# Optimization experiments

Measured on AMD Instinct MI355X. Metric: run time of the kernel, lower is better.

## Reference

```python
import jax, jax.numpy as jnp
import numpy as np
from jax import lax

WINDOW = 144
N_ROUNDS = 1
REDUCTION = 4
RES_SCALE = 0.1


def conv2d(x, w, b, pad):
    # x: (N,C,H,W), w: (O,I,kh,kw)
    out = lax.conv_general_dilated(x, w, (1, 1), [(pad, pad), (pad, pad)],
                                   dimension_numbers=('NCHW', 'OIHW', 'NCHW'))
    return out + b[None, :, None, None]


def l2norm(x, eps):
    # matches torch F.normalize: x / clamp_min(||x||, eps)
    n = jnp.sqrt(jnp.sum(x * x, axis=-1, keepdims=True))
    return x / jnp.maximum(n, eps)


def _adjacent(t):
    # t: (N, rounds, k, w, e) -> concat [self, roll+1, roll-1] along window dim
    back = jnp.roll(t, 1, axis=2)
    fwd = jnp.roll(t, -1, axis=2)
    return jnp.concatenate([t, back, fwd], axis=3)


def _forward(input_x, w_match, b_match, w_asm, b_asm, means):
    N, C, H, W = input_x.shape
    L = H * W
    Cr = C // REDUCTION
    x_embed = conv2d(input_x, w_match, b_match, 1).reshape(N, Cr, L).transpose(0, 2, 1)  # (N,L,Cr)
    y_embed = conv2d(input_x, w_asm, b_asm, 0).reshape(N, C, L).transpose(0, 2, 1)       # (N,L,C)

    # ---- k-means bucket routing (no-grad in original) ----
    xn = jnp.broadcast_to(l2norm(x_embed, 1e-12)[:, None], (N, N_ROUNDS, L, Cr))
    dists = jnp.einsum('bhld,hcd->bhlc', lax.stop_gradient(xn), means)
    buckets = jnp.argmax(dists, axis=-1)                      # (N, rounds, L)
    n_clusters = means.shape[1]
    offsets = (jnp.arange(N_ROUNDS) * n_clusters)[None, :, None]
    codes = (buckets + offsets).reshape(N, N_ROUNDS * L)

    # ---- sort tokens by bucket code, gather embeddings ----
    indices = jnp.argsort(codes, axis=-1)
    undo_sort = jnp.argsort(indices, axis=-1)
    mod_idx = indices % L
    x_sorted = jnp.take_along_axis(x_embed, mod_idx[..., None], axis=1)  # (N, r*L, Cr)
    y_sorted = jnp.take_along_axis(y_embed, mod_idx[..., None], axis=1)  # (N, r*L, C)

    padding = (WINDOW - L % WINDOW) % WINDOW
    xb = x_sorted.reshape(N, N_ROUNDS, L, Cr)
    yb = y_sorted.reshape(N, N_ROUNDS, L, C)
    if padding:
        xb = jnp.concatenate([xb, xb[:, :, -padding:, :]], axis=2)
        yb = jnp.concatenate([yb, yb[:, :, -padding:, :]], axis=2)
    k = xb.shape[2] // WINDOW
    xb = xb.reshape(N, N_ROUNDS, k, WINDOW, Cr)
    yb = yb.reshape(N, N_ROUNDS, k, WINDOW, C)

    # ---- windowed local attention over adjacent buckets ----
    x_match = _adjacent(l2norm(xb, 5e-5))   # (N,r,k,3w,Cr)  keys normalized
    y_adj = _adjacent(yb)                    # (N,r,k,3w,C)
    raw = jnp.einsum('bhkie,bhkje->bhkij', xb, x_match)   # (N,r,k,w,3w)
    lse = jax.nn.logsumexp(raw, axis=-1, keepdims=True)
    score = jnp.exp(raw - lse)
    ret = jnp.einsum('bhkij,bhkje->bhkie', score, y_adj)  # (N,r,k,w,C)

    ret = ret.reshape(N, N_ROUNDS, k * WINDOW, C)
    lse = lse.reshape(N, N_ROUNDS, k * WINDOW)
    if padding:
        ret = ret[:, :, :-padding, :]
        lse = lse[:, :, :-padding]
    ret = ret.reshape(N, N_ROUNDS * L, C)
    lse = lse.reshape(N, N_ROUNDS * L)

    # ---- undo sort, round-softmax combine ----
    ret = jnp.take_along_axis(ret, undo_sort[..., None], axis=1)
    lse = jnp.take_along_axis(lse, undo_sort, axis=1)
    ret = ret.reshape(N, N_ROUNDS, L, C)
    probs = jax.nn.softmax(lse.reshape(N, N_ROUNDS, L, 1), axis=1)
    ret = jnp.sum(ret * probs, axis=1)        # (N,L,C)
    return ret.transpose(0, 2, 1).reshape(N, C, H, W) * RES_SCALE + input_x


def setup_inputs() -> dict:
    key = jax.random.key(0)
    ks = jax.random.split(key, 6)
    N, C, H, W = 8, 256, 96, 96
    Cr = C // REDUCTION
    return {
        'input_x': jax.random.normal(ks[0], (N, C, H, W), jnp.float32),
        'w_match': jax.random.normal(ks[1], (Cr, C, 3, 3), jnp.float32) * 0.02,
        'b_match': jnp.zeros((Cr,), jnp.float32),
        'w_asm': jax.random.normal(ks[2], (C, C, 1, 1), jnp.float32) * 0.05,
        'b_asm': jnp.zeros((C,), jnp.float32),
        'means': l2norm(jax.random.normal(ks[3], (N_ROUNDS, 128, Cr), jnp.float32), 1e-12),
    }


def reference(input_x, w_match, b_match, w_asm, b_asm, means):
    return _forward(input_x, w_match, b_match, w_asm, b_asm, means)
```

## Files before the change

### kernel.cpp

```cpp
#include <hip/hip_runtime.h>
#include <math.h>

#define L 9216
#define HH 96
#define WW 96
#define CC 256
#define CR 64
#define NCLUST 128
#define WIN 144
#define NK 64

typedef float f32x4 __attribute__((ext_vector_type(4)));
typedef float f32x16 __attribute__((ext_vector_type(16)));
typedef short s8v __attribute__((ext_vector_type(8)));
typedef short s4v __attribute__((ext_vector_type(4)));

static __device__ __forceinline__ short f2bf(float x) {
  union { float f; unsigned u; } v; v.f = x;
  unsigned r = (v.u + 0x7FFF + ((v.u >> 16) & 1)) >> 16;
  return (short)r;
}
static __device__ __forceinline__ float bf2f(short h) {
  union { float f; unsigned u; } v;
  v.u = ((unsigned)(unsigned short)h) << 16;
  return v.f;
}

__global__ __launch_bounds__(256) void k_isplit(const float* __restrict__ in,
                                                unsigned short* __restrict__ xhi,
                                                unsigned short* __restrict__ xlo) {
  int h = blockIdx.x, icc = blockIdx.y, b = blockIdx.z;
  __shared__ float tile[16][97];
  int t = threadIdx.x;
  for (int e = t; e < 1536; e += 256) {
    int ic = e / 96, w = e % 96;
    tile[ic][w] = in[((size_t)(b * 256 + icc * 16 + ic)) * L + h * 96 + w];
  }
  __syncthreads();
  size_t base = (((size_t)b * 96 + h) * 16 + icc) * 1536;
  for (int e = t; e < 1536; e += 256) {
    int w = e >> 4, ic = e & 15;
    float v = tile[ic][w];
    short hi = f2bf(v);
    float rv = v - bf2f(hi);
    short lo = f2bf(rv);
    xhi[base + e] = (unsigned short)hi;
    xlo[base + e] = (unsigned short)lo;
  }
}

__global__ __launch_bounds__(256) void k_wsplit(const float* __restrict__ wm,
                                                unsigned short* __restrict__ whiB,
                                                unsigned short* __restrict__ wloB) {
  int idx = blockIdx.x * 256 + threadIdx.x;
  if (idx < 147456) {
    int ic = idx & 15;
    int oc = (idx >> 4) & 63;
    int g = idx >> 10;
    int tap = g % 9, icc = g / 9;
    float v = wm[(size_t)oc * 2304 + (icc * 16 + ic) * 9 + tap];
    short hi = f2bf(v);
    float rv = v - bf2f(hi);
    whiB[idx] = (unsigned short)hi;
    wloB[idx] = (unsigned short)f2bf(rv);
  }
}

__global__ __launch_bounds__(256) void k_w1prep(const float* __restrict__ wa,
                                                unsigned short* __restrict__ wt1) {
  int idx = blockIdx.x * 256 + threadIdx.x;
  int ic = idx & 15, oc = (idx >> 4) & 255, icc = idx >> 12;
  wt1[idx] = (unsigned short)f2bf(wa[(size_t)oc * 256 + icc * 16 + ic]);
}

__global__ __launch_bounds__(192) void k_conv3(const unsigned short* __restrict__ xhi,
                                               const unsigned short* __restrict__ xlo,
                                               const unsigned short* __restrict__ whiB,
                                               const unsigned short* __restrict__ wloB,
                                               const float* __restrict__ bm,
                                               float* __restrict__ xe) {
  int i = blockIdx.x;
  int b = i & 7, hp = i >> 3;
  int h0 = hp * 2;
  __shared__ __align__(16) unsigned short lds[25088];
  int t = threadIdx.x;
  int pt = t >> 6, lane = t & 63;
  int hh = lane >> 5, j = lane & 31;
  int r = lane & 31;

  for (int e = t; e < 512; e += 192) {
    int ic = e & 15, slot = e >> 4;
    int bs = slot >> 4, rem = slot & 15;
    int s = rem >> 3, rem2 = rem & 7;
    int rr = rem2 >> 1, cc = rem2 & 1;
    lds[bs * 12544 + s * 6272 + rr * 1568 + (cc ? 97 : 0) * 16 + ic] = 0;
  }

  f32x16 acc[4] = {};

  auto stage = [&](int icc, int buf) {
#pragma unroll
    for (int k8 = 0; k8 < 8; ++k8) {
      int u = t + k8 * 192;
      int s = u / 768;
      int rem = u - s * 768;
      int rr = rem / 192;
      int q = rem - rr * 192;
      int gr = h0 - 1 + rr;
      unsigned short* dst = &lds[buf * 12544 + s * 6272 + rr * 1568 + 16 + q * 8];
      if (gr >= 0 && gr < 96) {
        const unsigned short* src =
            (s ? xlo : xhi) + ((((size_t)b * 96 + gr) * 16 + icc) * 1536 + q * 8);
        __builtin_amdgcn_global_load_lds((const __attribute__((address_space(1))) void*)src,
                                         (__attribute__((address_space(3))) void*)dst, 16, 0, 0);
      } else {
        *(s8v*)dst = (s8v){0, 0, 0, 0, 0, 0, 0, 0};
      }
    }
  };

  auto compute = [&](int icc, int buf) {
    const unsigned short* lbase = lds + buf * 12544;
    const unsigned short* wb = whiB + (size_t)icc * 9216;
    const unsigned short* wl = wloB + (size_t)icc * 9216;
#pragma unroll
    for (int kh = 0; kh < 3; ++kh)
#pragma unroll
      for (int kw = 0; kw < 3; ++kw) {
        int tap = kh * 3 + kw;
        int woff = tap * 1024 + j * 16 + hh * 8;
        s8v b_hi0 = *(const s8v*)(wb + woff);
        s8v b_lo0 = *(const s8v*)(wl + woff);
        s8v b_hi1 = *(const s8v*)(wb + woff + 512);
        s8v b_lo1 = *(const s8v*)(wl + woff + 512);
#pragma unroll
        for (int rw = 0; rw < 2; ++rw) {
          int aidx = (rw + kh) * 1568 + (pt * 32 + r + kw) * 16 + hh * 8;
          s8v a_hi = *(const s8v*)(lbase + aidx);
          s8v a_lo = *(const s8v*)(lbase + 6272 + aidx);
          acc[rw * 2 + 0] = __builtin_amdgcn_mfma_f32_32x32x16_bf16(a_hi, b_hi0, acc[rw * 2 + 0], 0, 0, 0);
          acc[rw * 2 + 0] = __builtin_amdgcn_mfma_f32_32x32x16_bf16(a_hi, b_lo0, acc[rw * 2 + 0], 0, 0, 0);
          acc[rw * 2 + 0] = __builtin_amdgcn_mfma_f32_32x32x16_bf16(a_lo, b_hi0, acc[rw * 2 + 0], 0, 0, 0);
          acc[rw * 2 + 1] = __builtin_amdgcn_mfma_f32_32x32x16_bf16(a_hi, b_hi1, acc[rw * 2 + 1], 0, 0, 0);
          acc[rw * 2 + 1] = __builtin_amdgcn_mfma_f32_32x32x16_bf16(a_hi, b_lo1, acc[rw * 2 + 1], 0, 0, 0);
          acc[rw * 2 + 1] = __builtin_amdgcn_mfma_f32_32x32x16_bf16(a_lo, b_hi1, acc[rw * 2 + 1], 0, 0, 0);
        }
      }
  };

  stage(0, 0);
  __syncthreads();
#pragma unroll 1
  for (int icc = 0; icc < 16; ++icc) {
    int buf = icc & 1;
    if (icc < 15) stage(icc + 1, buf ^ 1);
    compute(icc, buf);
    __syncthreads();
  }

  float bv0 = bm[j], bv1 = bm[32 + j];
#pragma unroll
  for (int rw = 0; rw < 2; ++rw) {
#pragma unroll
    for (int reg = 0; reg < 16; ++reg) {
      int prow = (reg & 3) + 8 * (reg >> 2) + 4 * hh;
      size_t rowbase = ((size_t)b * L + (h0 + rw) * 96 + pt * 32 + prow) * 64;
      xe[rowbase + j] = acc[rw * 2 + 0][reg] + bv0;
      xe[rowbase + 32 + j] = acc[rw * 2 + 1][reg] + bv1;
    }
  }
}

__global__ __launch_bounds__(384) void k_conv1(const unsigned short* __restrict__ xhi,
                                               const unsigned short* __restrict__ wt1,
                                               const float* __restrict__ ba,
                                               unsigned short* __restrict__ yeb) {
  int h = blockIdx.x, b = blockIdx.y;
  int t = threadIdx.x;
  int wave = t >> 6, lane = t & 63;
  int pt = wave % 3, ot = wave / 3;
  int hh = lane >> 5, j = lane & 31;
  int r = lane & 31;

  f32x16 acc[4] = {};
  const unsigned short* abase =
      xhi + (((size_t)b * 96 + h) * 16) * 1536 + (pt * 32 + r) * 16 + hh * 8;
  const unsigned short* bbase = wt1 + (ot * 128 + j) * 16 + hh * 8;
#pragma unroll 2
  for (int icc = 0; icc < 16; ++icc) {
    s8v av = *(const s8v*)(abase + icc * 1536);
    const unsigned short* bp = bbase + icc * 4096;
#pragma unroll
    for (int tile = 0; tile < 4; ++tile) {
      s8v bv = *(const s8v*)(bp + tile * 512);
      acc[tile] = __builtin_amdgcn_mfma_f32_32x32x16_bf16(av, bv, acc[tile], 0, 0, 0);
    }
  }
#pragma unroll
  for (int tile = 0; tile < 4; ++tile) {
    int oc = ot * 128 + tile * 32 + j;
    float bias = ba[oc];
#pragma unroll
    for (int reg = 0; reg < 16; ++reg) {
      int prow = (reg & 3) + 8 * (reg >> 2) + 4 * hh;
      yeb[((size_t)b * L + h * 96 + pt * 32 + prow) * 256 + oc] =
          (unsigned short)f2bf(acc[tile][reg] + bias);
    }
  }
}

__global__ __launch_bounds__(256) void k_bucket(const float* __restrict__ xe,
                                                const float* __restrict__ means,
                                                int* __restrict__ buckets) {
  int lt = blockIdx.x, b = blockIdx.y;
  int l0 = lt * 32;
  __shared__ float x_s[32 * 65];
  __shared__ float m_s[128 * 65];
  __shared__ float bv_s[32 * 8];
  __shared__ int bi_s[32 * 8];
  int t = threadIdx.x;
  for (int e = t; e < 2048; e += 256) {
    int px = e >> 6, d = e & 63;
    x_s[px * 65 + d] = xe[((size_t)b * L + l0) * 64 + e];
  }
  for (int e = t; e < 8192; e += 256) {
    int c = e >> 6, d = e & 63;
    m_s[c * 65 + d] = means[e];
  }
  __syncthreads();
  int px = t >> 3, cg = t & 7;
  float best = -1e30f;
  int bidx = 0;
  const float* xr = &x_s[px * 65];
  for (int cc = 0; cc < 16; ++cc) {
    int c = cg + 8 * cc;
    const float* mr = &m_s[c * 65];
    float d = 0.f;
#pragma unroll
    for (int dd = 0; dd < 64; ++dd) d += xr[dd] * mr[dd];
    if (d > best || (d == best && c < bidx)) { best = d; bidx = c; }
  }
  bv_s[px * 8 + cg] = best;
  bi_s[px * 8 + cg] = bidx;
  __syncthreads();
  if (cg == 0) {
    float bb = bv_s[px * 8];
    int bbi = bi_s[px * 8];
    for (int g = 1; g < 8; ++g) {
      float v = bv_s[px * 8 + g];
      int vi = bi_s[px * 8 + g];
      if (v > bb || (v == bb && vi < bbi)) { bb = v; bbi = vi; }
    }
    buckets[b * L + l0 + px] = bbi;
  }
}

#define SCH 256
#define CHL 36
__global__ __launch_bounds__(256) void k_sort(const int* __restrict__ buckets,
                                              int* __restrict__ sidx) {
  int b = blockIdx.x, t = threadIdx.x;
  __shared__ int keys_s[L];
  __shared__ unsigned short cnt_s[SCH][130];
  __shared__ int halfsum0[NCLUST];
  __shared__ int keytotal[NCLUST];
  __shared__ int keybase[NCLUST];
  const int* bk = buckets + b * L;
  for (int i = t; i < L; i += SCH) keys_s[i] = bk[i];
  for (int i = 0; i < 130; ++i) cnt_s[t][i] = 0;
  __syncthreads();
  {
    int base = t * CHL;
    for (int i = 0; i < CHL; ++i) cnt_s[t][keys_s[base + i]]++;
  }
  __syncthreads();
  {
    int kkey = t & 127, h = t >> 7;
    int c0 = h * 128;
    int run = 0;
    for (int c = 0; c < 128; ++c) {
      int v = cnt_s[c0 + c][kkey];
      cnt_s[c0 + c][kkey] = (unsigned short)run;
      run += v;
    }
    if (h == 0) halfsum0[kkey] = run;
    else keytotal[kkey] = run;
  }
  __syncthreads();
  if (t < NCLUST) keytotal[t] += halfsum0[t];
  __syncthreads();
  if (t == 0) {
    int s = 0;
    for (int i = 0; i < NCLUST; ++i) { keybase[i] = s; s += keytotal[i]; }
  }
  __syncthreads();
  {
    int h = t >> 7;
    int base = t * CHL;
    int* sb = sidx + b * L;
    for (int i = 0; i < CHL; ++i) {
      int kkey = keys_s[base + i];
      int pos = keybase[kkey] + (h ? halfsum0[kkey] : 0) + cnt_s[t][kkey];
      cnt_s[t][kkey]++;
      sb[pos] = base + i;
    }
  }
}

__global__ __launch_bounds__(256) void k_gather(const float* __restrict__ xe,
                                                const unsigned short* __restrict__ yeb,
                                                const int* __restrict__ sidx,
                                                unsigned short* __restrict__ xk,
                                                unsigned short* __restrict__ yt,
                                                float* __restrict__ norms) {
  int it = blockIdx.x, b = blockIdx.y;
  int i0 = it * 64;
  __shared__ float x_s[64 * 65];
  __shared__ unsigned short y_s[16 * 260];
  __shared__ int idx_s[64];
  __shared__ float scale_s[64];
  int t = threadIdx.x;
  if (t < 64) idx_s[t] = sidx[b * L + i0 + t];
  __syncthreads();
  for (int e = t; e < 4096; e += 256) {
    int i = e >> 6, d = e & 63;
    x_s[i * 65 + d] = xe[((size_t)b * L + idx_s[i]) * 64 + d];
  }
  __syncthreads();
  if (t < 64) {
    float s = 0.f;
    const float* xr = &x_s[t * 65];
#pragma unroll
    for (int d = 0; d < 64; ++d) s += xr[d] * xr[d];
    float n = fmaxf(sqrtf(s), 5e-5f);
    norms[b * L + i0 + t] = n;
    scale_s[t] = 1.0f / n;
  }
  __syncthreads();
  for (int e = t; e < 4096; e += 256) {
    int i = e >> 6, d = e & 63;
    int ig = i0 + i;
    int db = (((d >> 3) ^ (ig & 7)) << 3) | (d & 7);
    xk[((size_t)b * L + ig) * 64 + db] = (unsigned short)f2bf(x_s[i * 65 + d] * scale_s[i]);
  }
  for (int tile = 0; tile < 4; ++tile) {
    for (int e = t; e < 4096; e += 256) {
      int i16 = e >> 8, c = e & 255;
      y_s[i16 * 260 + c] = yeb[((size_t)b * L + idx_s[tile * 16 + i16]) * 256 + c];
    }
    __syncthreads();
    size_t tb = (size_t)b * L * 256 + (size_t)((i0 >> 4) + tile) * 4096;
    for (int e = t; e < 4096; e += 256) {
      int c = e >> 4, k16 = e & 15;
      int sw = ((((k16 >> 2) ^ ((c >> 2) & 3)) << 2) | (k16 & 3));
      yt[tb + c * 16 + sw] = y_s[k16 * 260 + c];
    }
    __syncthreads();
  }
}

__global__ __launch_bounds__(576, 1) void k_attn(const unsigned short* __restrict__ xk,
                                                 const unsigned short* __restrict__ yt,
                                                 const float* __restrict__ norms,
                                                 const int* __restrict__ sidx,
                                                 float* __restrict__ retb) {
  int i = blockIdx.x;
  int b = i & 7, k = i >> 3;
  __shared__ __align__(16) char lds[40960];
  int t = threadIdx.x;
  int lane = t & 63;
  int g = lane >> 4, kr = lane & 15;
  int kbase = k * WIN;
  int qr0 = kbase + (t >> 6) * 16;
  int qrow = qr0 + kr;

  s8v qf[2];
#pragma unroll
  for (int s = 0; s < 2; ++s) {
    int blk = (4 * s + g) ^ (qrow & 7);
    qf[s] = *(const s8v*)(xk + ((size_t)b * L + qrow) * 64 + blk * 8);
  }
  float qn = norms[(size_t)b * L + qrow];

  f32x4 acc[16];
#pragma unroll
  for (int nf = 0; nf < 16; ++nf) acc[nf] = (f32x4){0.f, 0.f, 0.f, 0.f};
  float runm = -3e38f, runsum = 0.f;

  auto stage = [&](int c, int buf) {
    char* kb = lds + buf * 20480;
    char* vb = kb + 4096;
    for (int e = t; e < 1280; e += 576) {
      if (e < 256) {
        int key32 = e >> 3;
        if (c == 13 && key32 >= 16) continue;
        int j = c * 32 + key32;
        int r = (j >= 288) ? 2 : (j >= 144) ? 1 : 0;
        int kk = (r == 0) ? k : (r == 1) ? ((k + 63) & 63) : ((k + 1) & 63);
        int phys = kk * WIN + (j - r * 144);
        const char* gp = (const char*)xk + (((size_t)b * L + phys) * 64 + (e & 7) * 8) * 2;
        __builtin_amdgcn_global_load_lds((const __attribute__((address_space(1))) void*)gp,
                                         (__attribute__((address_space(3))) void*)(kb + e * 16),
                                         16, 0, 0);
      } else {
        int u = e - 256;
        int f = u >> 9;
        if (c == 13 && f == 1) continue;
        int j0 = c * 32 + f * 16;
        int r = (j0 >= 288) ? 2 : (j0 >= 144) ? 1 : 0;
        int kk = (r == 0) ? k : (r == 1) ? ((k + 63) & 63) : ((k + 1) & 63);
        int rowbase = kk * WIN + (j0 - r * 144);
        const char* gp = (const char*)yt + ((size_t)b * L + rowbase) * 512 + (size_t)(u & 511) * 16;
        __builtin_amdgcn_global_load_lds((const __attribute__((address_space(1))) void*)gp,
                                         (__attribute__((address_space(3))) void*)(vb + u * 16),
                                         16, 0, 0);
      }
    }
  };

  auto compute = [&](int c, int buf) {
    char* kb = lds + buf * 20480;
    char* vb = kb + 4096;
    int nm = (c == 13) ? 1 : 2;
    f32x4 sa[2];
    sa[0] = (f32x4){0.f, 0.f, 0.f, 0.f};
    sa[1] = (f32x4){0.f, 0.f, 0.f, 0.f};
#pragma unroll
    for (int m = 0; m < 2; ++m)
      if (m < nm) {
        int row32 = m * 16 + kr;
#pragma unroll
        for (int s = 0; s < 2; ++s) {
          int off = row32 * 128 + (((4 * s + g) ^ (row32 & 7)) * 16);
          s8v kf = *(const s8v*)(kb + off);
          sa[m] = __builtin_amdgcn_mfma_f32_16x16x32_bf16(kf, qf[s], sa[m], 0, 0, 0);
        }
      }
    float p[2][4];
    float mx = -3e38f;
#pragma unroll
    for (int m = 0; m < 2; ++m)
#pragma unroll
      for (int r = 0; r < 4; ++r) {
        float v = (m < nm) ? sa[m][r] * qn : -3e38f;
        p[m][r] = v;
        mx = fmaxf(mx, v);
      }
    mx = fmaxf(mx, __shfl_xor(mx, 16));
    mx = fmaxf(mx, __shfl_xor(mx, 32));
    if (!__all(mx <= runm + 8.f)) {
      float newm = fmaxf(runm, mx);
      float corr = __expf(runm - newm);
      runm = newm;
      runsum *= corr;
      float f0 = __shfl(corr, 4 * g + 0);
      float f1 = __shfl(corr, 4 * g + 1);
      float f2 = __shfl(corr, 4 * g + 2);
      float f3 = __shfl(corr, 4 * g + 3);
#pragma unroll
      for (int nf = 0; nf < 16; ++nf) {
        acc[nf][0] *= f0; acc[nf][1] *= f1; acc[nf][2] *= f2; acc[nf][3] *= f3;
      }
    }
    float psum = 0.f;
#pragma unroll
    for (int m = 0; m < 2; ++m)
#pragma unroll
      for (int r = 0; r < 4; ++r) {
        float pv = __expf(p[m][r] - runm);
        p[m][r] = pv;
        psum += pv;
      }
    runsum += psum;
    s8v pa;
#pragma unroll
    for (int e2 = 0; e2 < 8; ++e2) pa[e2] = f2bf(p[e2 >> 2][e2 & 3]);
#pragma unroll
    for (int nf = 0; nf < 16; ++nf) {
      int cch = nf * 16 + kr;
      int grp = g ^ ((cch >> 2) & 3);
      s4v lo = *(const s4v*)(vb + cch * 32 + grp * 8);
      s4v hi = *(const s4v*)(vb + 8192 + cch * 32 + grp * 8);
      s8v bfv = __builtin_shufflevector(lo, hi, 0, 1, 2, 3, 4, 5, 6, 7);
      acc[nf] = __builtin_amdgcn_mfma_f32_16x16x32_bf16(pa, bfv, acc[nf], 0, 0, 0);
    }
  };

  stage(0, 0);
  __syncthreads();
  for (int c = 0; c < 14; ++c) {
    if (c < 13) stage(c + 1, (c + 1) & 1);
    compute(c, c & 1);
    __syncthreads();
  }

  runsum += __shfl_xor(runsum, 16);
  runsum += __shfl_xor(runsum, 32);
  float inv = 1.0f / runsum;
  float invr[4];
  int lorig[4];
#pragma unroll
  for (int r = 0; r < 4; ++r) {
    invr[r] = __shfl(inv, 4 * g + r);
    lorig[r] = sidx[b * L + qr0 + 4 * g + r];
  }
#pragma unroll
  for (int nf = 0; nf < 16; ++nf)
#pragma unroll
    for (int r = 0; r < 4; ++r)
      retb[((size_t)b * L + lorig[r]) * 256 + nf * 16 + kr] = acc[nf][r] * invr[r];
}

__global__ __launch_bounds__(256) void k_final(const float* __restrict__ in,
                                               const float* __restrict__ retb,
                                               float* __restrict__ out) {
  int lt = blockIdx.x, ct = blockIdx.y, b = blockIdx.z;
  int l0 = lt * 32, c0 = ct * 32;
  __shared__ float t_s[32][33];
  int t = threadIdx.x;
  for (int e = t; e < 1024; e += 256) {
    int i = e >> 5, j = e & 31;
    t_s[i][j] = retb[((size_t)b * L + l0 + i) * 256 + c0 + j];
  }
  __syncthreads();
  for (int e = t; e < 1024; e += 256) {
    int ci = e >> 5, lj = e & 31;
    size_t o = ((size_t)b * CC + c0 + ci) * L + l0 + lj;
    out[o] = in[o] + 0.1f * t_s[lj][ci];
  }
}

extern "C" void kernel_launch(void* const* d_in, const int* in_sizes, int n_in,
                              void* d_out, int out_size, void* d_ws, size_t ws_size,
                              hipStream_t stream) {
  const float* input = (const float*)d_in[0];
  const float* wm = (const float*)d_in[1];
  const float* bm = (const float*)d_in[2];
  const float* wa = (const float*)d_in[3];
  const float* ba = (const float*)d_in[4];
  const float* means = (const float*)d_in[5];
  float* out = (float*)d_out;

  float* ws = (float*)d_ws;
  float* x_embed = ws;
  float* y_embed = ws + 4718592ull;
  float* retb = y_embed;
  unsigned short* xk = (unsigned short*)(ws + 23592960ull);
  unsigned short* yt = (unsigned short*)(ws + 25952256ull);
  float* norms = ws + 35389440ull;
  int* buckets = (int*)(ws + 35463168ull);
  int* sidx = buckets + 73728;
  unsigned short* xhi = (unsigned short*)y_embed;
  unsigned short* xlo = xhi + 18874368ull;
  unsigned short* yeb = xlo;
  unsigned short* whiB = xk;
  unsigned short* wloB = whiB + 294912ull;
  unsigned short* wt1 = wloB + 294912ull;

  k_isplit<<<dim3(96, 16, 8), 256, 0, stream>>>(input, xhi, xlo);
  k_wsplit<<<dim3(576), 256, 0, stream>>>(wm, whiB, wloB);
  k_w1prep<<<dim3(256), 256, 0, stream>>>(wa, wt1);
  k_conv3<<<dim3(384), 192, 0, stream>>>(xhi, xlo, whiB, wloB, bm, x_embed);
  k_conv1<<<dim3(96, 8), 384, 0, stream>>>(xhi, wt1, ba, yeb);
  k_bucket<<<dim3(288, 8), 256, 0, stream>>>(x_embed, means, buckets);
  k_sort<<<dim3(8), 256, 0, stream>>>(buckets, sidx);
  k_gather<<<dim3(144, 8), 256, 0, stream>>>(x_embed, yeb, sidx, xk, yt, norms);
  k_attn<<<dim3(512), 576, 0, stream>>>(xk, yt, norms, sidx, retb);
  k_final<<<dim3(288, 8, 8), 256, 0, stream>>>(input, retb, out);
}
```

Measured before the change: 314.7 us.

## Split 3x3 conv input channels across two blocks with a reduction pass

The 3x3 match conv grid is doubled by splitting the 16 input-channel chunks into two halves, each handled by its own block. One half writes to x_embed with bias and the other writes partial sums to a scratch buffer. A new vectorized kernel then adds the two. The aim is to fill more CUs, since 384 blocks underuse the MI355X, at the cost of an extra partial-output write, a read-add-write pass and one more launch.

```diff
diff --git a/kernel.cpp b/kernel.cpp
--- a/kernel.cpp
+++ b/kernel.cpp
@@ -78,10 +78,14 @@
                                                const unsigned short* __restrict__ whiB,
                                                const unsigned short* __restrict__ wloB,
                                                const float* __restrict__ bm,
-                                               float* __restrict__ xe) {
+                                               float* __restrict__ xe,
+                                               float* __restrict__ xpart) {
   int i = blockIdx.x;
-  int b = i & 7, hp = i >> 3;
+  int b = i & 7;
+  int v = i >> 3;
+  int hp = v % 48, ich = v / 48;
   int h0 = hp * 2;
+  int icc0 = ich * 8;
   __shared__ __align__(16) unsigned short lds[25088];
   int t = threadIdx.x;
   int pt = t >> 6, lane = t & 63;
@@ -148,26 +152,38 @@
       }
   };
 
-  stage(0, 0);
+  stage(icc0, 0);
   __syncthreads();
 #pragma unroll 1
-  for (int icc = 0; icc < 16; ++icc) {
-    int buf = icc & 1;
-    if (icc < 15) stage(icc + 1, buf ^ 1);
-    compute(icc, buf);
+  for (int c = 0; c < 8; ++c) {
+    int buf = c & 1;
+    if (c < 7) stage(icc0 + c + 1, buf ^ 1);
+    compute(icc0 + c, buf);
     __syncthreads();
   }
 
-  float bv0 = bm[j], bv1 = bm[32 + j];
+  float* dst = ich ? xpart : xe;
+  float bv0 = ich ? 0.f : bm[j];
+  float bv1 = ich ? 0.f : bm[32 + j];
 #pragma unroll
   for (int rw = 0; rw < 2; ++rw) {
 #pragma unroll
     for (int reg = 0; reg < 16; ++reg) {
       int prow = (reg & 3) + 8 * (reg >> 2) + 4 * hh;
       size_t rowbase = ((size_t)b * L + (h0 + rw) * 96 + pt * 32 + prow) * 64;
-      xe[rowbase + j] = acc[rw * 2 + 0][reg] + bv0;
-      xe[rowbase + 32 + j] = acc[rw * 2 + 1][reg] + bv1;
-    }
+      dst[rowbase + j] = acc[rw * 2 + 0][reg] + bv0;
+      dst[rowbase + 32 + j] = acc[rw * 2 + 1][reg] + bv1;
+    }
+  }
+}
+
+__global__ __launch_bounds__(256) void k_xred(float* __restrict__ xe,
+                                              const float* __restrict__ xpart) {
+  int idx = blockIdx.x * 256 + threadIdx.x;
+  if (idx < 1179648) {
+    f32x4 a = *(const f32x4*)&xe[idx * 4];
+    a += *(const f32x4*)&xpart[idx * 4];
+    *(f32x4*)&xe[idx * 4] = a;
   }
 }
 
@@ -556,11 +572,13 @@
   unsigned short* whiB = xk;
   unsigned short* wloB = whiB + 294912ull;
   unsigned short* wt1 = wloB + 294912ull;
+  float* xpart = ws + 25952256ull;
 
   k_isplit<<<dim3(96, 16, 8), 256, 0, stream>>>(input, xhi, xlo);
   k_wsplit<<<dim3(576), 256, 0, stream>>>(wm, whiB, wloB);
   k_w1prep<<<dim3(256), 256, 0, stream>>>(wa, wt1);
-  k_conv3<<<dim3(384), 192, 0, stream>>>(xhi, xlo, whiB, wloB, bm, x_embed);
+  k_conv3<<<dim3(768), 192, 0, stream>>>(xhi, xlo, whiB, wloB, bm, x_embed, xpart);
+  k_xred<<<dim3(4608), 256, 0, stream>>>(x_embed, xpart);
   k_conv1<<<dim3(96, 8), 384, 0, stream>>>(xhi, wt1, ba, yeb);
   k_bucket<<<dim3(288, 8), 256, 0, stream>>>(x_embed, means, buckets);
   k_sort<<<dim3(8), 256, 0, stream>>>(buckets, sidx);
```

Result: slower. 321.7 us (+2.2%).
